# Optimization experiments

Measured on AMD Instinct MI355X. Metric: run time of the kernel, lower is better.

The kernel has to match this reference:

```python
import jax, jax.numpy as jnp
import numpy as np

B, L, V, E, H = 64, 256, 256, 256, 1024

def setup_inputs() -> dict:
    key = jax.random.key(0)
    ks = jax.random.split(key, 7)
    inputs = jax.random.randint(ks[0], (B, L), 0, V, dtype=jnp.int32)
    embedding = jax.random.normal(ks[1], (V, E), dtype=jnp.float32)  # stddev=1.0 per emb_init
    # GRU weights: input projections (no bias) and hidden projections (with bias),
    # concatenated over gates [r, z, n].
    Wi = jax.random.normal(ks[2], (E, 3 * H), dtype=jnp.float32) / np.sqrt(E)
    Wh = jax.random.normal(ks[3], (H, 3 * H), dtype=jnp.float32) / np.sqrt(H)
    bh = jnp.zeros((3 * H,), dtype=jnp.float32)
    # Output dense (xavier_uniform-like scale)
    lim = np.sqrt(6.0 / (H + V))
    Wout = jax.random.uniform(ks[4], (H, V), dtype=jnp.float32, minval=-lim, maxval=lim)
    bout = jax.random.normal(ks[5], (V,), dtype=jnp.float32) * 1e-6
    return {"inputs": inputs, "embedding": embedding, "Wi": Wi, "Wh": Wh,
            "bh": bh, "Wout": Wout, "bout": bout}

def reference(inputs, embedding, Wi, Wh, bh, Wout, bout):
    # Embedding lookup: [B, L] -> [B, L, E]
    x = jnp.take(embedding, inputs, axis=0)
    # Precompute input-side gate projections for all timesteps (batched GEMM).
    xw = jnp.einsum('ble,ef->blf', x, Wi)  # [B, L, 3H]
    hidden = Wh.shape[0]

    def step(h, xw_t):
        gh = h @ Wh + bh                       # [B, 3H]
        xr, xz, xn = jnp.split(xw_t, 3, axis=-1)
        hr, hz, hn = jnp.split(gh, 3, axis=-1)
        r = jax.nn.sigmoid(xr + hr)
        z = jax.nn.sigmoid(xz + hz)
        n = jnp.tanh(xn + r * hn)
        h_new = (1.0 - z) * n + z * h          # GRUCell update
        return h_new, h_new

    h0 = jnp.zeros((x.shape[0], hidden), dtype=x.dtype)
    _, ys = jax.lax.scan(step, h0, jnp.swapaxes(xw, 0, 1))  # scan over time
    y = jnp.swapaxes(ys, 0, 1)                 # [B, L, H]
    logits = jnp.einsum('blh,hv->blv', y, Wout) + bout
    return logits
```

## Files before the change

kernel.cpp:

```cpp
#include <hip/hip_runtime.h>
#include <cstdint>
#include <math.h>

#define B_  64
#define L_  256
#define V_  256
#define E_  256
#define H_  1024
#define H3  3072

typedef __bf16 bf16x8 __attribute__((ext_vector_type(8)));
typedef float  f32x4  __attribute__((ext_vector_type(4)));

__device__ __forceinline__ unsigned short f2bf(float f) {
    union { float f; unsigned u; } v; v.f = f;
    unsigned r = v.u + 0x7fffu + ((v.u >> 16) & 1u);
    return (unsigned short)(r >> 16);
}

__device__ __forceinline__ int chunk_ok(bf16x8 v) {
    union { bf16x8 b; unsigned u[4]; } cv; cv.b = v;
    int ok = 1;
#pragma unroll
    for (int i = 0; i < 4; i++) {
        unsigned x = cv.u[i] ^ 0xAAAAAAAAu;
        ok &= (int)((x & 0xFFFFu) != 0u) & (int)((x >> 16) != 0u);
    }
    return ok;
}

__device__ __forceinline__ float sigmoid_f(float x) {
    return __builtin_amdgcn_rcpf(1.0f + __expf(-x));
}
__device__ __forceinline__ float tanh_f(float x) {
    return 1.0f - 2.0f * __builtin_amdgcn_rcpf(1.0f + __expf(2.0f * x));
}

__global__ __launch_bounds__(256) void prep_all(
        const float* __restrict__ Wh, const float* __restrict__ Wi,
        const float* __restrict__ Wout, const float* __restrict__ emb,
        unsigned short* __restrict__ WhT, unsigned short* __restrict__ WiT,
        unsigned short* __restrict__ WoutT, unsigned short* __restrict__ embB,
        unsigned short* __restrict__ h0b, uint4* __restrict__ poison) {
    __shared__ unsigned short tile[32][34];
    int bid = blockIdx.x;
    const float* src; unsigned short* dst; int rows, cols, nt, kt;
    if (bid < 3072)      { src = Wh;   dst = WhT;   rows = H_; cols = H3; nt = bid % 96; kt = bid / 96; }
    else if (bid < 3840) { int b = bid - 3072; src = Wi;   dst = WiT;   rows = E_; cols = H3; nt = b % 96; kt = b / 96; }
    else if (bid < 4096) { int b = bid - 3840; src = Wout; dst = WoutT; rows = H_; cols = V_; nt = b % 8;  kt = b / 8; }
    else if (bid < 4352) {
        int idx = (bid - 4096) * 256 + threadIdx.x;
        embB[idx] = f2bf(emb[idx]);
        h0b[idx]  = 0;
        return;
    } else {
        size_t T = (size_t)(bid - 4352) * 256 + threadIdx.x;
        uint4 v; v.x = v.y = v.z = v.w = 0xAAAAAAAAu;
        poison[T] = v;
        return;
    }
    int n0 = nt * 32, k0 = kt * 32;
    int tx = threadIdx.x & 31, ty = threadIdx.x >> 5;
#pragma unroll
    for (int j = 0; j < 32; j += 8)
        tile[tx][ty + j] = f2bf(src[(size_t)(k0 + ty + j) * cols + (n0 + tx)]);
    __syncthreads();
#pragma unroll
    for (int j = 0; j < 32; j += 8)
        dst[(size_t)(n0 + ty + j) * rows + (k0 + tx)] = tile[ty + j][tx];
}

__global__ __launch_bounds__(256, 1) void gru_persistent(
        unsigned short* __restrict__ hist,
        const unsigned short* __restrict__ WhT,
        const unsigned short* __restrict__ WiT,
        const unsigned short* __restrict__ embB,
        const int* __restrict__ tokens,
        const float* __restrict__ bh) {
    __shared__ f32x4 red[2][4][4][64];

    int bid = blockIdx.x;
    int btile = bid & 3;
    int jtile = bid >> 2;
    int wave = threadIdx.x >> 6, lane = threadIdx.x & 63;
    int l16 = lane & 15, q = lane >> 4;
    int b0 = btile * 16, j0 = jtile * 16;
    int kbase = wave * 256;

    bf16x8 Wreg[3][8];
#pragma unroll
    for (int g = 0; g < 3; g++) {
        const bf16x8* Brow = (const bf16x8*)(WhT + (size_t)(g * H_ + j0 + l16) * H_);
#pragma unroll
        for (int kk = 0; kk < 8; kk++) {
            Wreg[g][kk] = Brow[(kbase >> 3) + kk * 4 + q];
            asm volatile("" : "+v"(Wreg[g][kk]));
        }
    }
    bf16x8 Wxreg[3][2];
#pragma unroll
    for (int g = 0; g < 3; g++) {
        const bf16x8* Bx = (const bf16x8*)(WiT + (size_t)(g * H_ + j0 + l16) * E_);
#pragma unroll
        for (int c = 0; c < 2; c++) {
            Wxreg[g][c] = Bx[wave * 8 + c * 4 + q];
            asm volatile("" : "+v"(Wxreg[g][c]));
        }
    }

    int Lp  = threadIdx.x & 63;
    int reg = threadIdx.x >> 6;
    int b_local = (Lp >> 4) * 4 + reg;
    int j_local = Lp & 15;
    int b = b0 + b_local, jg = j0 + j_local;
    float bhr = bh[jg];
    float bhz = bh[H_ + jg];
    float bhn = bh[2 * H_ + jg];
    asm volatile("" : "+v"(bhr), "+v"(bhz), "+v"(bhn));
    float hreg = 0.0f;

    const int tokrow = (b0 + l16) * L_;

    for (int t = 0; t < L_; t++) {
        const unsigned short* hist_t  = hist + (size_t)t * (B_ * H_);
        unsigned short*       hist_t1 = hist + (size_t)(t + 1) * (B_ * H_);

        int tok = tokens[tokrow + t];
        const bf16x8* Ax = (const bf16x8*)(embB + (size_t)tok * E_);
        bf16x8 ax0 = Ax[wave * 8 + q];
        bf16x8 ax1 = Ax[wave * 8 + 4 + q];
        f32x4 xaccR = {}, xaccZ = {}, xaccN = {};
        xaccR = __builtin_amdgcn_mfma_f32_16x16x32_bf16(ax0, Wxreg[0][0], xaccR, 0, 0, 0);
        xaccR = __builtin_amdgcn_mfma_f32_16x16x32_bf16(ax1, Wxreg[0][1], xaccR, 0, 0, 0);
        xaccZ = __builtin_amdgcn_mfma_f32_16x16x32_bf16(ax0, Wxreg[1][0], xaccZ, 0, 0, 0);
        xaccZ = __builtin_amdgcn_mfma_f32_16x16x32_bf16(ax1, Wxreg[1][1], xaccZ, 0, 0, 0);
        xaccN = __builtin_amdgcn_mfma_f32_16x16x32_bf16(ax0, Wxreg[2][0], xaccN, 0, 0, 0);
        xaccN = __builtin_amdgcn_mfma_f32_16x16x32_bf16(ax1, Wxreg[2][1], xaccN, 0, 0, 0);

        const unsigned short* p = hist_t + (size_t)(b0 + l16) * H_ + kbase + q * 8;
        bf16x8 a0, a1, a2, a3, a4, a5, a6, a7;

        {
            int spins = 0;
            while (true) {
                asm volatile("global_load_dwordx4 %0, %1, off sc0 sc1" : "=v"(a0) : "v"(p));
                asm volatile("global_load_dwordx4 %0, %1, off sc0 sc1" : "=v"(a1) : "v"(p + 32));
                asm volatile("global_load_dwordx4 %0, %1, off sc0 sc1" : "=v"(a2) : "v"(p + 64));
                asm volatile("global_load_dwordx4 %0, %1, off sc0 sc1" : "=v"(a3) : "v"(p + 96));
                asm volatile("s_waitcnt vmcnt(0)"
                             : "+v"(a0), "+v"(a1), "+v"(a2), "+v"(a3) :: "memory");
                int ok = chunk_ok(a0) & chunk_ok(a1) & chunk_ok(a2) & chunk_ok(a3);
                if (__all(ok)) break;
                if (++spins > (1 << 18)) break;
                __builtin_amdgcn_s_sleep(1);
            }
        }
        asm volatile("global_load_dwordx4 %0, %1, off sc0 sc1" : "=v"(a4) : "v"(p + 128));
        asm volatile("global_load_dwordx4 %0, %1, off sc0 sc1" : "=v"(a5) : "v"(p + 160));
        asm volatile("global_load_dwordx4 %0, %1, off sc0 sc1" : "=v"(a6) : "v"(p + 192));
        asm volatile("global_load_dwordx4 %0, %1, off sc0 sc1" : "=v"(a7) : "v"(p + 224));

        f32x4 acc[3];
        acc[0] = xaccR; acc[1] = xaccZ; acc[2] = (f32x4){};
#pragma unroll
        for (int g = 0; g < 3; g++) {
            acc[g] = __builtin_amdgcn_mfma_f32_16x16x32_bf16(a0, Wreg[g][0], acc[g], 0, 0, 0);
            acc[g] = __builtin_amdgcn_mfma_f32_16x16x32_bf16(a1, Wreg[g][1], acc[g], 0, 0, 0);
            acc[g] = __builtin_amdgcn_mfma_f32_16x16x32_bf16(a2, Wreg[g][2], acc[g], 0, 0, 0);
            acc[g] = __builtin_amdgcn_mfma_f32_16x16x32_bf16(a3, Wreg[g][3], acc[g], 0, 0, 0);
        }

        asm volatile("s_waitcnt vmcnt(0)"
                     : "+v"(a4), "+v"(a5), "+v"(a6), "+v"(a7) :: "memory");
        {
            int ok = chunk_ok(a4) & chunk_ok(a5) & chunk_ok(a6) & chunk_ok(a7);
            if (!__all(ok)) {
                int spins = 0;
                while (true) {
                    __builtin_amdgcn_s_sleep(1);
                    asm volatile("global_load_dwordx4 %0, %1, off sc0 sc1" : "=v"(a4) : "v"(p + 128));
                    asm volatile("global_load_dwordx4 %0, %1, off sc0 sc1" : "=v"(a5) : "v"(p + 160));
                    asm volatile("global_load_dwordx4 %0, %1, off sc0 sc1" : "=v"(a6) : "v"(p + 192));
                    asm volatile("global_load_dwordx4 %0, %1, off sc0 sc1" : "=v"(a7) : "v"(p + 224));
                    asm volatile("s_waitcnt vmcnt(0)"
                                 : "+v"(a4), "+v"(a5), "+v"(a6), "+v"(a7) :: "memory");
                    int ok2 = chunk_ok(a4) & chunk_ok(a5) & chunk_ok(a6) & chunk_ok(a7);
                    if (__all(ok2)) break;
                    if (++spins > (1 << 18)) break;
                }
            }
        }
#pragma unroll
        for (int g = 0; g < 3; g++) {
            acc[g] = __builtin_amdgcn_mfma_f32_16x16x32_bf16(a4, Wreg[g][4], acc[g], 0, 0, 0);
            acc[g] = __builtin_amdgcn_mfma_f32_16x16x32_bf16(a5, Wreg[g][5], acc[g], 0, 0, 0);
            acc[g] = __builtin_amdgcn_mfma_f32_16x16x32_bf16(a6, Wreg[g][6], acc[g], 0, 0, 0);
            acc[g] = __builtin_amdgcn_mfma_f32_16x16x32_bf16(a7, Wreg[g][7], acc[g], 0, 0, 0);
        }

        int par = t & 1;
#pragma unroll
        for (int g = 0; g < 3; g++)
            red[par][wave][g][lane] = acc[g];
        red[par][wave][3][lane] = xaccN;
        __syncthreads();

        float s0 = red[par][0][0][Lp][reg] + red[par][1][0][Lp][reg] + red[par][2][0][Lp][reg] + red[par][3][0][Lp][reg];
        float s1 = red[par][0][1][Lp][reg] + red[par][1][1][Lp][reg] + red[par][2][1][Lp][reg] + red[par][3][1][Lp][reg];
        float s2 = red[par][0][2][Lp][reg] + red[par][1][2][Lp][reg] + red[par][2][2][Lp][reg] + red[par][3][2][Lp][reg];
        float s3 = red[par][0][3][Lp][reg] + red[par][1][3][Lp][reg] + red[par][2][3][Lp][reg] + red[par][3][3][Lp][reg];

        float r = sigmoid_f(s0 + bhr);
        float z = sigmoid_f(s1 + bhz);
        float n = tanh_f(s3 + r * (s2 + bhn));
        float hnew = n + z * (hreg - n);
        hreg = hnew;

        unsigned short hbv = f2bf(hnew);
        if (hbv == 0xAAAAu) hbv = 0xAAABu;

        {
            unsigned short* hp = hist_t1 + (size_t)b * H_ + jg;
            unsigned hv32 = hbv;
            asm volatile("global_store_short %0, %1, off sc0 sc1"
                         :: "v"(hp), "v"(hv32) : "memory");
        }
    }
}

__global__ __launch_bounds__(256) void out_gemm(const unsigned short* __restrict__ hist,
                                                const unsigned short* __restrict__ WoutT,
                                                const float* __restrict__ bout,
                                                float* __restrict__ out) {
    int ntile = blockIdx.x;
    int mtile = blockIdx.y;
    int wave = threadIdx.x >> 6, lane = threadIdx.x & 63;
    int l16 = lane & 15, q = lane >> 4;

    int m = mtile * 64 + wave * 16 + l16;
    int bb = m >> 8, tt = m & 255;
    const bf16x8* Arow = (const bf16x8*)(hist + (size_t)(tt + 1) * (B_ * H_) + (size_t)bb * H_);
    int n0 = ntile * 64;

    f32x4 acc[4] = {};
    for (int k0 = 0; k0 < H_; k0 += 32) {
        bf16x8 a = Arow[(k0 >> 3) + q];
#pragma unroll
        for (int j = 0; j < 4; j++) {
            const bf16x8* Brow = (const bf16x8*)(WoutT + (size_t)(n0 + j*16 + l16) * H_);
            bf16x8 b = Brow[(k0 >> 3) + q];
            acc[j] = __builtin_amdgcn_mfma_f32_16x16x32_bf16(a, b, acc[j], 0, 0, 0);
        }
    }
    int mrow = mtile * 64 + wave * 16 + q * 4;
#pragma unroll
    for (int j = 0; j < 4; j++) {
        int n = n0 + j * 16 + l16;
        float bias = bout[n];
#pragma unroll
        for (int r = 0; r < 4; r++)
            out[(size_t)(mrow + r) * V_ + n] = acc[j][r] + bias;
    }
}

extern "C" void kernel_launch(void* const* d_in, const int* in_sizes, int n_in,
                              void* d_out, int out_size, void* d_ws, size_t ws_size,
                              hipStream_t stream) {
    const int*   tokens = (const int*)  d_in[0];
    const float* emb    = (const float*)d_in[1];
    const float* Wi     = (const float*)d_in[2];
    const float* Wh     = (const float*)d_in[3];
    const float* bh     = (const float*)d_in[4];
    const float* Wout   = (const float*)d_in[5];
    const float* bout   = (const float*)d_in[6];
    float* out = (float*)d_out;

    char* ws = (char*)d_ws;
    size_t off = 0;
    auto alloc = [&](size_t bytes) -> void* {
        void* p = ws + off;
        off += (bytes + 255) & ~(size_t)255;
        return p;
    };
    unsigned short* WhT   = (unsigned short*)alloc((size_t)H3 * H_ * 2);
    unsigned short* WiT   = (unsigned short*)alloc((size_t)H3 * E_ * 2);
    unsigned short* WoutT = (unsigned short*)alloc((size_t)V_ * H_ * 2);
    unsigned short* embB  = (unsigned short*)alloc((size_t)V_ * E_ * 2);
    unsigned short* hist  = (unsigned short*)alloc((size_t)(L_ + 1) * B_ * H_ * 2);

    prep_all<<<12544, 256, 0, stream>>>(Wh, Wi, Wout, emb, WhT, WiT, WoutT,
                                        embB, hist, (uint4*)(hist + (size_t)B_ * H_));

    {
        unsigned short* ah = hist;
        const unsigned short* aW = WhT; const unsigned short* aWx = WiT;
        const unsigned short* ae = embB; const int* at = tokens;
        const float* ab = bh;
        void* args[] = {&ah, &aW, &aWx, &ae, &at, &ab};
        hipError_t err = hipLaunchCooperativeKernel((void*)gru_persistent,
                                                    dim3(256), dim3(256), args, 0, stream);
        if (err != hipSuccess) {
            gru_persistent<<<dim3(256), dim3(256), 0, stream>>>(
                ah, aW, aWx, ae, at, ab);
        }
    }

    out_gemm<<<dim3(4, 256), 256, 0, stream>>>(hist, WoutT, bout, out);
}
```

Baseline: 865.4 us.

## Fuse output projection GEMM into persistent GRU kernel tail

Removes the separate out_gemm launch and runs the output projection at the end of the persistent GRU kernel. Each block computes 64 output rows across all four column tiles. Only blocks whose rows include the final timestep spin-wait, with a sentinel check on the last hidden state, before reading it. The aim is to save a kernel launch and let the GEMM start while other blocks finish the recurrence. In exchange, each block now covers four times the GEMM work that a single out_gemm block did, and the spin-wait has a bounded timeout fallback.

Result: slower. 885.2 us (+2.3%).

```diff
diff --git a/kernel.cpp b/kernel.cpp
--- a/kernel.cpp
+++ b/kernel.cpp
@@ -11,6 +11,7 @@
 
 typedef __bf16 bf16x8 __attribute__((ext_vector_type(8)));
 typedef float  f32x4  __attribute__((ext_vector_type(4)));
+typedef unsigned u32x2 __attribute__((ext_vector_type(2)));
 
 __device__ __forceinline__ unsigned short f2bf(float f) {
     union { float f; unsigned u; } v; v.f = f;
@@ -76,7 +77,10 @@
         const unsigned short* __restrict__ WiT,
         const unsigned short* __restrict__ embB,
         const int* __restrict__ tokens,
-        const float* __restrict__ bh) {
+        const float* __restrict__ bh,
+        const unsigned short* __restrict__ WoutT,
+        const float* __restrict__ bout,
+        float* __restrict__ out) {
     __shared__ f32x4 red[2][4][4][64];
 
     int bid = blockIdx.x;
@@ -226,40 +230,52 @@
                          :: "v"(hp), "v"(hv32) : "memory");
         }
     }
-}
-
-__global__ __launch_bounds__(256) void out_gemm(const unsigned short* __restrict__ hist,
-                                                const unsigned short* __restrict__ WoutT,
-                                                const float* __restrict__ bout,
-                                                float* __restrict__ out) {
-    int ntile = blockIdx.x;
-    int mtile = blockIdx.y;
-    int wave = threadIdx.x >> 6, lane = threadIdx.x & 63;
-    int l16 = lane & 15, q = lane >> 4;
-
-    int m = mtile * 64 + wave * 16 + l16;
-    int bb = m >> 8, tt = m & 255;
-    const bf16x8* Arow = (const bf16x8*)(hist + (size_t)(tt + 1) * (B_ * H_) + (size_t)bb * H_);
-    int n0 = ntile * 64;
-
-    f32x4 acc[4] = {};
-    for (int k0 = 0; k0 < H_; k0 += 32) {
-        bf16x8 a = Arow[(k0 >> 3) + q];
-#pragma unroll
-        for (int j = 0; j < 4; j++) {
-            const bf16x8* Brow = (const bf16x8*)(WoutT + (size_t)(n0 + j*16 + l16) * H_);
-            bf16x8 b = Brow[(k0 >> 3) + q];
-            acc[j] = __builtin_amdgcn_mfma_f32_16x16x32_bf16(a, b, acc[j], 0, 0, 0);
-        }
-    }
-    int mrow = mtile * 64 + wave * 16 + q * 4;
-#pragma unroll
-    for (int j = 0; j < 4; j++) {
-        int n = n0 + j * 16 + l16;
-        float bias = bout[n];
-#pragma unroll
-        for (int r = 0; r < 4; r++)
-            out[(size_t)(mrow + r) * V_ + n] = acc[j][r] + bias;
+
+    if ((bid & 3) == 3) {
+        const unsigned short* hp = hist + (size_t)L_ * (B_ * H_)
+                                 + (size_t)(bid >> 2) * H_ + threadIdx.x * 4;
+        int spins = 0;
+        while (true) {
+            u32x2 v;
+            asm volatile("global_load_dwordx2 %0, %1, off sc0 sc1" : "=v"(v) : "v"(hp));
+            asm volatile("s_waitcnt vmcnt(0)" : "+v"(v) :: "memory");
+            unsigned x0 = v[0], x1 = v[1];
+            int ok = (int)((x0 & 0xFFFFu) != 0xAAAAu) & (int)((x0 >> 16) != 0xAAAAu)
+                   & (int)((x1 & 0xFFFFu) != 0xAAAAu) & (int)((x1 >> 16) != 0xAAAAu);
+            if (ok) break;
+            if (++spins > (1 << 18)) break;
+            __builtin_amdgcn_s_sleep(1);
+        }
+    }
+    __syncthreads();
+
+    {
+        int m  = bid * 64 + wave * 16 + l16;
+        int bb = m >> 8, tt = m & 255;
+        const bf16x8* Arow = (const bf16x8*)(hist + (size_t)(tt + 1) * (B_ * H_)
+                                                  + (size_t)bb * H_);
+        int mrow = bid * 64 + wave * 16 + q * 4;
+        for (int ntile = 0; ntile < 4; ntile++) {
+            int n0 = ntile * 64;
+            f32x4 oacc[4] = {};
+            for (int k0 = 0; k0 < H_; k0 += 32) {
+                bf16x8 a = Arow[(k0 >> 3) + q];
+#pragma unroll
+                for (int j = 0; j < 4; j++) {
+                    const bf16x8* Brow = (const bf16x8*)(WoutT + (size_t)(n0 + j * 16 + l16) * H_);
+                    bf16x8 bf = Brow[(k0 >> 3) + q];
+                    oacc[j] = __builtin_amdgcn_mfma_f32_16x16x32_bf16(a, bf, oacc[j], 0, 0, 0);
+                }
+            }
+#pragma unroll
+            for (int j = 0; j < 4; j++) {
+                int n = n0 + j * 16 + l16;
+                float bias = bout[n];
+#pragma unroll
+                for (int r2 = 0; r2 < 4; r2++)
+                    out[(size_t)(mrow + r2) * V_ + n] = oacc[j][r2] + bias;
+            }
+        }
     }
 }
 
@@ -296,14 +312,14 @@
         const unsigned short* aW = WhT; const unsigned short* aWx = WiT;
         const unsigned short* ae = embB; const int* at = tokens;
         const float* ab = bh;
-        void* args[] = {&ah, &aW, &aWx, &ae, &at, &ab};
+        const unsigned short* aWo = WoutT; const float* abo = bout;
+        float* ao = out;
+        void* args[] = {&ah, &aW, &aWx, &ae, &at, &ab, &aWo, &abo, &ao};
         hipError_t err = hipLaunchCooperativeKernel((void*)gru_persistent,
                                                     dim3(256), dim3(256), args, 0, stream);
         if (err != hipSuccess) {
             gru_persistent<<<dim3(256), dim3(256), 0, stream>>>(
-                ah, aW, aWx, ae, at, ab);
-        }
-    }
-
-    out_gemm<<<dim3(4, 256), 256, 0, stream>>>(hist, WoutT, bout, out);
-}
+                ah, aW, aWx, ae, at, ab, aWo, abo, ao);
+        }
+    }
+}
```
